# Performance work log

Hardware: AMD Instinct MI355X
Metric: run time of the kernel (lower is better)

## Reference

```python
import jax, jax.numpy as jnp
import numpy as np

N_TOK, EMBED, N_CLS, BATCH, N_HEAD = 32768, 512, 16, 8, 8
D_HEAD = EMBED // N_HEAD


def setup_inputs() -> dict:
    key0 = jax.random.key(0)
    ks = jax.random.split(key0, 12)
    s = 1.0 / np.sqrt(EMBED)
    query = jax.random.normal(ks[0], (N_TOK, EMBED), dtype=jnp.float32)
    key_f = jax.random.normal(ks[1], (N_CLS, BATCH, EMBED), dtype=jnp.float32)
    val_f = jax.random.normal(ks[2], (N_CLS, BATCH, EMBED), dtype=jnp.float32)
    batch_idx = jnp.sort(jax.random.randint(ks[3], (N_TOK,), 0, BATCH)).astype(jnp.int32)
    Wq = jax.random.normal(ks[4], (EMBED, EMBED), dtype=jnp.float32) * s
    bq = jnp.zeros((EMBED,), dtype=jnp.float32)
    Wk = jax.random.normal(ks[5], (EMBED, EMBED), dtype=jnp.float32) * s  # Conv1d(k=1) kernel squeezed
    bk = jnp.zeros((EMBED,), dtype=jnp.float32)
    Wv = jax.random.normal(ks[6], (EMBED, EMBED), dtype=jnp.float32) * s
    bv = jnp.zeros((EMBED,), dtype=jnp.float32)
    Wo = jax.random.normal(ks[7], (EMBED, EMBED), dtype=jnp.float32) * s
    bo = jnp.zeros((EMBED,), dtype=jnp.float32)
    return {"query": query, "key": key_f, "value": val_f, "batch_idx": batch_idx,
            "batch_size": BATCH, "Wq": Wq, "bq": bq, "Wk": Wk, "bk": bk,
            "Wv": Wv, "bv": bv, "Wo": Wo, "bo": bo}


def reference(query, key, value, batch_idx, batch_size, Wq, bq, Wk, bk, Wv, bv, Wo, bo):
    n_tok, embed = query.shape
    L, B, _ = key.shape
    H, D = N_HEAD, EMBED // N_HEAD
    scale = D ** -0.5  # matmul_norm
    # projections (Conv1d with kernel_size=1 == pointwise linear over E)
    q = (query @ Wq.T + bq).reshape(n_tok, H, D)                           # [N,H,D]
    k = (jnp.einsum('lbe,fe->blf', key, Wk) + bk)                          # [B,L,E]
    k = k.transpose(0, 2, 1).reshape(B, H, D, L)                           # [B,H,D,L]
    v = (jnp.einsum('lbe,fe->blf', value, Wv) + bv)                        # [B,L,E]
    v = v.transpose(0, 2, 1).reshape(B, H, D, L).transpose(0, 1, 3, 2)     # [B,H,L,D]
    # scores against every batch's prototypes, then pick each token's batch
    scores_all = jnp.einsum('nhd,bhdl->nbhl', q, k) * scale                # [N,B,H,L]
    sel = batch_idx.astype(jnp.int32)[:, None, None, None]
    scores = jnp.take_along_axis(scores_all, sel, axis=1).squeeze(1)       # [N,H,L]
    p = jax.nn.softmax(scores, axis=-1)
    ctx_all = jnp.einsum('nhl,bhld->nbhd', p, v)                           # [N,B,H,D]
    ctx = jnp.take_along_axis(ctx_all, sel, axis=1).squeeze(1)             # [N,H,D]
    return ctx.reshape(n_tok, embed) @ Wo.T + bo
```

## Files before the change

kernel.cpp:

```cpp
#include <hip/hip_runtime.h>

typedef unsigned short u16;
typedef __attribute__((ext_vector_type(8))) short short8;
typedef __attribute__((ext_vector_type(4))) unsigned short u16x4;
typedef __attribute__((ext_vector_type(4))) float f32x4;

#define N_TOKENS 32768
#define EMBED 512
#define NCLS 16
#define NBATCH 8
#define NHEAD 8
#define DHEAD 64

__device__ __forceinline__ u16 f2bf(float f) {
  unsigned u = __float_as_uint(f);
  u += 0x7fffu + ((u >> 16) & 1u);
  return (u16)(u >> 16);
}

__device__ __forceinline__ void async16(const u16* g, u16* l) {
  __builtin_amdgcn_global_load_lds(
      (__attribute__((address_space(1))) const unsigned int*)(const void*)g,
      (__attribute__((address_space(3))) unsigned int*)(void*)l,
      16, 0, 0);
}

__global__ __launch_bounds__(256) void kvproj_kernel(
    const float* __restrict__ key, const float* __restrict__ val,
    const float* __restrict__ Wk, const float* __restrict__ bk,
    const float* __restrict__ Wv, const float* __restrict__ bv,
    float* __restrict__ kproj, float* __restrict__ vproj) {
  int t = blockIdx.x * blockDim.x + threadIdx.x;
  int o = t >> 1;
  int half = t & 1;
  const bool isV = o >= 65536;
  int idx = o & 65535;
  int f = idx & 511;
  int bl = idx >> 9;
  int l = bl & 15;
  int b = bl >> 4;
  const float* src = isV ? val : key;
  const float* W = isV ? Wv : Wk;
  const float* bias = isV ? bv : bk;
  const float4* s4 = (const float4*)(src + (size_t)l * (NBATCH * EMBED) + (size_t)b * EMBED) + half * 64;
  const float4* w4 = (const float4*)(W + (size_t)f * EMBED) + half * 64;
  float acc = 0.f;
#pragma unroll 8
  for (int e = 0; e < 64; e++) {
    float4 a = s4[e], w = w4[e];
    acc += a.x * w.x + a.y * w.y + a.z * w.z + a.w * w.w;
  }
  acc += __shfl_xor(acc, 1);
  if (half == 0) {
    acc += bias[f];
    if (!isV) {
      kproj[((size_t)(b * EMBED + f)) * NCLS + l] = acc;
    } else {
      int h = f >> 6, d = f & 63;
      vproj[(size_t)b * 8192 + (size_t)h * 1024 + l * 64 + d] = acc;
    }
  }
}

__global__ __launch_bounds__(256) void build_all(
    const float* __restrict__ kproj, const float* __restrict__ vproj,
    const float* __restrict__ Wq, const float* __restrict__ bq,
    const float* __restrict__ Wo,
    u16* __restrict__ Kqb, u16* __restrict__ WoVb, float* __restrict__ sb) {
  const int blk = blockIdx.x;
  if (blk < 2048) {
    int t = blk * 256 + threadIdx.x;
    int e = t & 511;
    int hl = (t >> 9) & 127;
    int b = t >> 16;
    int h = hl >> 4, l = hl & 15;
    const float* kp = kproj + (size_t)b * 8192 + h * 1024 + l;
    const float* wq = Wq + (size_t)(h * 64) * 512 + e;
    float acc = 0.f;
#pragma unroll 16
    for (int d = 0; d < 64; d++) acc += kp[d * 16] * wq[d * 512];
    Kqb[t] = f2bf(acc);
  } else if (blk < 4096) {
    int t = (blk - 2048) * 256 + threadIdx.x;
    int hl = t & 127;
    int f = (t >> 7) & 511;
    int b = t >> 16;
    int h = hl >> 4, l = hl & 15;
    const float* vp = vproj + (size_t)b * 8192 + h * 1024 + l * 64;
    const float* wo = Wo + (size_t)f * 512 + h * 64;
    float acc = 0.f;
#pragma unroll 16
    for (int d = 0; d < 64; d++) acc += vp[d] * wo[d];
    WoVb[t] = f2bf(acc);
  } else {
    int t = (blk - 4096) * 256 + threadIdx.x;
    int hl = t & 127, b = t >> 7;
    int h = hl >> 4, l = hl & 15;
    const float* kp = kproj + (size_t)b * 8192 + h * 1024 + l;
    const float* q = bq + h * 64;
    float acc = 0.f;
#pragma unroll
    for (int d = 0; d < 64; d++) acc += q[d] * kp[d * 16];
    sb[t] = acc;
  }
}

__global__ __launch_bounds__(256) void fused_attn(
    const float* __restrict__ query, const u16* __restrict__ Kqb,
    const u16* __restrict__ WoVb, const float* __restrict__ sb,
    const float* __restrict__ bo, const int* __restrict__ bidx,
    float* __restrict__ out) {
  __shared__ __align__(16) u16 Bs[2][128 * 32];
  __shared__ __align__(16) u16 Ps[64 * 128];
  const int tid = threadIdx.x;
  const int lane = tid & 63;
  const int wave = tid >> 6;
  const int quad = lane >> 4;
  const int l16 = lane & 15;
  const int tileId = blockIdx.x >> 1;
  const int slot = blockIdx.x & 1;
  const int m0 = tileId * 64;
  const int bFirst = bidx[m0];
  const int bLast = bidx[m0 + 63];
  if (slot == 1 && bFirst == bLast) return;
  const int b0 = (slot == 0) ? bFirst : bFirst + 1;
  const int b1 = (slot == 0) ? bFirst : bLast;

  const int r0 = tid >> 2, r1 = r0 + 64;
  const int lg0 = (tid & 3) ^ ((r0 >> 1) & 3);
  const int lg1 = (tid & 3) ^ ((r1 >> 1) & 3);
  const size_t boff0 = (size_t)r0 * 512 + lg0 * 8;
  const size_t boff1 = (size_t)r1 * 512 + lg1 * 8;

  int rowb[4][4];
#pragma unroll
  for (int mi = 0; mi < 4; mi++)
#pragma unroll
    for (int r = 0; r < 4; r++) rowb[mi][r] = bidx[m0 + mi * 16 + quad * 4 + r];

  const float* pA = query + (size_t)(m0 + wave * 16 + l16) * 512 + quad * 8;

  for (int bb = b0; bb <= b1; bb++) {
    const u16* Bq = Kqb + (size_t)bb * 65536;

    async16(Bq + boff0, &Bs[0][tid * 8]);
    async16(Bq + boff1, &Bs[0][tid * 8 + 2048]);
    float4 na0 = *(const float4*)(pA);
    float4 na1 = *(const float4*)(pA + 4);

    f32x4 acc1[8];
#pragma unroll
    for (int j = 0; j < 8; j++) acc1[j] = (f32x4){0.f, 0.f, 0.f, 0.f};

    for (int t = 0; t < 16; t++) {
      __syncthreads();
      const int cur = t & 1;
      if (t < 15) {
        const int ko = (t + 1) * 32;
        async16(Bq + boff0 + ko, &Bs[cur ^ 1][tid * 8]);
        async16(Bq + boff1 + ko, &Bs[cur ^ 1][tid * 8 + 2048]);
      }
      float4 a0 = na0, a1 = na1;
      if (t < 15) {
        na0 = *(const float4*)(pA + (t + 1) * 32);
        na1 = *(const float4*)(pA + (t + 1) * 32 + 4);
      }
      short8 af;
      af[0] = (short)f2bf(a0.x); af[1] = (short)f2bf(a0.y);
      af[2] = (short)f2bf(a0.z); af[3] = (short)f2bf(a0.w);
      af[4] = (short)f2bf(a1.x); af[5] = (short)f2bf(a1.y);
      af[6] = (short)f2bf(a1.z); af[7] = (short)f2bf(a1.w);
#pragma unroll
      for (int ni = 0; ni < 8; ni++) {
        const int rw = ni * 16 + l16;
        short8 bfr = *(const short8*)&Bs[cur][rw * 32 + ((quad ^ ((rw >> 1) & 3)) << 3)];
        acc1[ni] = __builtin_amdgcn_mfma_f32_16x16x32_bf16(af, bfr, acc1[ni], 0, 0, 0);
      }
    }

    float sbv[8];
#pragma unroll
    for (int ni = 0; ni < 8; ni++) sbv[ni] = sb[bb * 128 + ni * 16 + l16];
#pragma unroll
    for (int r = 0; r < 4; r++) {
      const int row = wave * 16 + quad * 4 + r;
#pragma unroll
      for (int ni = 0; ni < 8; ni++) {
        float v = acc1[ni][r] + sbv[ni];
        float mx = v;
        mx = fmaxf(mx, __shfl_xor(mx, 1));
        mx = fmaxf(mx, __shfl_xor(mx, 2));
        mx = fmaxf(mx, __shfl_xor(mx, 4));
        mx = fmaxf(mx, __shfl_xor(mx, 8));
        float ev = __expf((v - mx) * 0.125f);
        float s = ev;
        s += __shfl_xor(s, 1);
        s += __shfl_xor(s, 2);
        s += __shfl_xor(s, 4);
        s += __shfl_xor(s, 8);
        const int col = ni * 16 + l16;
        Ps[row * 128 + (((col >> 3) ^ (row & 7)) << 3) + (col & 7)] = f2bf(ev / s);
      }
    }
    __syncthreads();

    const u16* Wv = WoVb + (size_t)bb * 65536;
#pragma unroll
    for (int h2 = 0; h2 < 2; h2++) {
      const int f0 = wave * 128 + h2 * 64;
      f32x4 acc2[4][4];
#pragma unroll
      for (int i = 0; i < 4; i++)
#pragma unroll
        for (int j = 0; j < 4; j++) acc2[i][j] = (f32x4){0.f, 0.f, 0.f, 0.f};
#pragma unroll
      for (int kk = 0; kk < 4; kk++) {
        short8 paf[4], bf2[4];
#pragma unroll
        for (int mi = 0; mi < 4; mi++) {
          const int row = mi * 16 + l16;
          paf[mi] = *(const short8*)&Ps[row * 128 + (((kk * 4 + quad) ^ (row & 7)) << 3)];
        }
#pragma unroll
        for (int ni = 0; ni < 4; ni++) {
          const int fr = f0 + ni * 16 + l16;
          bf2[ni] = *(const short8*)(Wv + (size_t)fr * 128 + kk * 32 + quad * 8);
        }
#pragma unroll
        for (int mi = 0; mi < 4; mi++)
#pragma unroll
          for (int ni = 0; ni < 4; ni++)
            acc2[mi][ni] = __builtin_amdgcn_mfma_f32_16x16x32_bf16(paf[mi], bf2[ni], acc2[mi][ni], 0, 0, 0);
      }
      float bov[4];
#pragma unroll
      for (int ni = 0; ni < 4; ni++) bov[ni] = bo[f0 + ni * 16 + l16];
#pragma unroll
      for (int mi = 0; mi < 4; mi++)
#pragma unroll
        for (int r = 0; r < 4; r++) {
          if (rowb[mi][r] == bb) {
            const size_t row = m0 + mi * 16 + quad * 4 + r;
#pragma unroll
            for (int ni = 0; ni < 4; ni++)
              out[row * 512 + f0 + ni * 16 + l16] = acc2[mi][ni][r] + bov[ni];
          }
        }
    }
    __syncthreads();
  }
}

extern "C" void kernel_launch(void* const* d_in, const int* in_sizes, int n_in,
                              void* d_out, int out_size, void* d_ws, size_t ws_size,
                              hipStream_t stream) {
  const float* query = (const float*)d_in[0];
  const float* keyt = (const float*)d_in[1];
  const float* valt = (const float*)d_in[2];
  const int* bidx = (const int*)d_in[3];
  const float* Wq = (const float*)d_in[5];
  const float* bq = (const float*)d_in[6];
  const float* Wk = (const float*)d_in[7];
  const float* bk = (const float*)d_in[8];
  const float* Wv = (const float*)d_in[9];
  const float* bv = (const float*)d_in[10];
  const float* Wo = (const float*)d_in[11];
  const float* bo = (const float*)d_in[12];
  float* out = (float*)d_out;

  unsigned char* w = (unsigned char*)d_ws;
  float* kproj = (float*)(w + 41943040ull);
  float* vproj = (float*)(w + 42205184ull);
  u16* Kqb = (u16*)(w + 42467328ull);
  u16* WoVb = (u16*)(w + 43515904ull);
  float* sb = (float*)(w + 44564480ull);

  kvproj_kernel<<<1024, 256, 0, stream>>>(keyt, valt, Wk, bk, Wv, bv, kproj, vproj);

  build_all<<<4100, 256, 0, stream>>>(kproj, vproj, Wq, bq, Wo, Kqb, WoVb, sb);

  fused_attn<<<N_TOKENS / 64 * 2, 256, 0, stream>>>(query, Kqb, WoVb, sb, bo, bidx, out);
}
```

Baseline: 277.3 us.

## Load Kq fragments directly from global, rework K/V projection and WoV build reductions

```diff
diff --git a/kernel.cpp b/kernel.cpp
--- a/kernel.cpp
+++ b/kernel.cpp
@@ -18,46 +18,42 @@
   return (u16)(u >> 16);
 }
 
-__device__ __forceinline__ void async16(const u16* g, u16* l) {
-  __builtin_amdgcn_global_load_lds(
-      (__attribute__((address_space(1))) const unsigned int*)(const void*)g,
-      (__attribute__((address_space(3))) unsigned int*)(void*)l,
-      16, 0, 0);
-}
-
 __global__ __launch_bounds__(256) void kvproj_kernel(
     const float* __restrict__ key, const float* __restrict__ val,
     const float* __restrict__ Wk, const float* __restrict__ bk,
     const float* __restrict__ Wv, const float* __restrict__ bv,
     float* __restrict__ kproj, float* __restrict__ vproj) {
-  int t = blockIdx.x * blockDim.x + threadIdx.x;
-  int o = t >> 1;
-  int half = t & 1;
-  const bool isV = o >= 65536;
-  int idx = o & 65535;
-  int f = idx & 511;
-  int bl = idx >> 9;
-  int l = bl & 15;
-  int b = bl >> 4;
+  const int tid = threadIdx.x;
+  const bool isV = blockIdx.x & 1;
+  const int fgrp = blockIdx.x >> 1;
+  const int wave = tid >> 6;
+  const int ec = tid & 63;
+  const int fr = fgrp * 4 + wave;
+  const float* W = (isV ? Wv : Wk) + (size_t)fr * 512 + ec * 8;
+  const float4 w0 = *(const float4*)W;
+  const float4 w1 = *(const float4*)(W + 4);
   const float* src = isV ? val : key;
-  const float* W = isV ? Wv : Wk;
-  const float* bias = isV ? bv : bk;
-  const float4* s4 = (const float4*)(src + (size_t)l * (NBATCH * EMBED) + (size_t)b * EMBED) + half * 64;
-  const float4* w4 = (const float4*)(W + (size_t)f * EMBED) + half * 64;
-  float acc = 0.f;
-#pragma unroll 8
-  for (int e = 0; e < 64; e++) {
-    float4 a = s4[e], w = w4[e];
-    acc += a.x * w.x + a.y * w.y + a.z * w.z + a.w * w.w;
-  }
-  acc += __shfl_xor(acc, 1);
-  if (half == 0) {
-    acc += bias[f];
-    if (!isV) {
-      kproj[((size_t)(b * EMBED + f)) * NCLS + l] = acc;
-    } else {
-      int h = f >> 6, d = f & 63;
-      vproj[(size_t)b * 8192 + (size_t)h * 1024 + l * 64 + d] = acc;
+  const float bval = (isV ? bv : bk)[fr];
+  const int h = fr >> 6, d = fr & 63;
+
+#pragma unroll 4
+  for (int r = 0; r < 128; r++) {
+    const int b = r >> 4, l = r & 15;
+    const float* s = src + (size_t)l * (NBATCH * EMBED) + (size_t)b * EMBED + ec * 8;
+    float4 a0 = *(const float4*)s;
+    float4 a1 = *(const float4*)(s + 4);
+    float acc = a0.x * w0.x + a0.y * w0.y + a0.z * w0.z + a0.w * w0.w +
+                a1.x * w1.x + a1.y * w1.y + a1.z * w1.z + a1.w * w1.w;
+    acc += __shfl_xor(acc, 1);
+    acc += __shfl_xor(acc, 2);
+    acc += __shfl_xor(acc, 4);
+    acc += __shfl_xor(acc, 8);
+    acc += __shfl_xor(acc, 16);
+    acc += __shfl_xor(acc, 32);
+    if (ec == 0) {
+      acc += bval;
+      if (!isV) kproj[((size_t)(b * EMBED + fr)) * NCLS + l] = acc;
+      else      vproj[(size_t)b * 8192 + (size_t)h * 1024 + l * 64 + d] = acc;
     }
   }
 }
@@ -80,20 +76,32 @@
 #pragma unroll 16
     for (int d = 0; d < 64; d++) acc += kp[d * 16] * wq[d * 512];
     Kqb[t] = f2bf(acc);
-  } else if (blk < 4096) {
-    int t = (blk - 2048) * 256 + threadIdx.x;
-    int hl = t & 127;
-    int f = (t >> 7) & 511;
-    int b = t >> 16;
-    int h = hl >> 4, l = hl & 15;
-    const float* vp = vproj + (size_t)b * 8192 + h * 1024 + l * 64;
-    const float* wo = Wo + (size_t)f * 512 + h * 64;
-    float acc = 0.f;
-#pragma unroll 16
-    for (int d = 0; d < 64; d++) acc += vp[d] * wo[d];
-    WoVb[t] = f2bf(acc);
+  } else if (blk < 3072) {
+    const int wave = threadIdx.x >> 6;
+    const int lane = threadIdx.x & 63;
+    const int wgid = (blk - 2048) * 4 + wave;
+    const int b = wgid >> 9, f = wgid & 511;
+    const int l = lane >> 2, c = lane & 3;
+    const float* vp = vproj + (size_t)b * 8192 + l * 64 + c * 16;
+    const float* wo = Wo + (size_t)f * 512 + c * 16;
+#pragma unroll 2
+    for (int h = 0; h < 8; h++) {
+      const float* v = vp + h * 1024;
+      const float* w = wo + h * 64;
+      float4 v0 = *(const float4*)v,       w0 = *(const float4*)w;
+      float4 v1 = *(const float4*)(v + 4), w1 = *(const float4*)(w + 4);
+      float4 v2 = *(const float4*)(v + 8), w2 = *(const float4*)(w + 8);
+      float4 v3 = *(const float4*)(v + 12), w3 = *(const float4*)(w + 12);
+      float acc = v0.x * w0.x + v0.y * w0.y + v0.z * w0.z + v0.w * w0.w +
+                  v1.x * w1.x + v1.y * w1.y + v1.z * w1.z + v1.w * w1.w +
+                  v2.x * w2.x + v2.y * w2.y + v2.z * w2.z + v2.w * w2.w +
+                  v3.x * w3.x + v3.y * w3.y + v3.z * w3.z + v3.w * w3.w;
+      acc += __shfl_xor(acc, 1);
+      acc += __shfl_xor(acc, 2);
+      if (c == 0) WoVb[(size_t)b * 65536 + (size_t)f * 128 + h * 16 + l] = f2bf(acc);
+    }
   } else {
-    int t = (blk - 4096) * 256 + threadIdx.x;
+    int t = (blk - 3072) * 256 + threadIdx.x;
     int hl = t & 127, b = t >> 7;
     int h = hl >> 4, l = hl & 15;
     const float* kp = kproj + (size_t)b * 8192 + h * 1024 + l;
@@ -110,7 +118,6 @@
     const u16* __restrict__ WoVb, const float* __restrict__ sb,
     const float* __restrict__ bo, const int* __restrict__ bidx,
     float* __restrict__ out) {
-  __shared__ __align__(16) u16 Bs[2][128 * 32];
   __shared__ __align__(16) u16 Ps[64 * 128];
   const int tid = threadIdx.x;
   const int lane = tid & 63;
@@ -126,12 +133,6 @@
   const int b0 = (slot == 0) ? bFirst : bFirst + 1;
   const int b1 = (slot == 0) ? bFirst : bLast;
 
-  const int r0 = tid >> 2, r1 = r0 + 64;
-  const int lg0 = (tid & 3) ^ ((r0 >> 1) & 3);
-  const int lg1 = (tid & 3) ^ ((r1 >> 1) & 3);
-  const size_t boff0 = (size_t)r0 * 512 + lg0 * 8;
-  const size_t boff1 = (size_t)r1 * 512 + lg1 * 8;
-
   int rowb[4][4];
 #pragma unroll
   for (int mi = 0; mi < 4; mi++)
@@ -141,40 +142,42 @@
   const float* pA = query + (size_t)(m0 + wave * 16 + l16) * 512 + quad * 8;
 
   for (int bb = b0; bb <= b1; bb++) {
-    const u16* Bq = Kqb + (size_t)bb * 65536;
-
-    async16(Bq + boff0, &Bs[0][tid * 8]);
-    async16(Bq + boff1, &Bs[0][tid * 8 + 2048]);
-    float4 na0 = *(const float4*)(pA);
-    float4 na1 = *(const float4*)(pA + 4);
+    const u16* Bq = Kqb + (size_t)bb * 65536 + (size_t)l16 * 512 + quad * 8;
 
     f32x4 acc1[8];
 #pragma unroll
     for (int j = 0; j < 8; j++) acc1[j] = (f32x4){0.f, 0.f, 0.f, 0.f};
 
+    short8 bc[8];
+#pragma unroll
+    for (int ni = 0; ni < 8; ni++)
+      bc[ni] = *(const short8*)(Bq + (size_t)ni * 16 * 512);
+    float4 a0c = *(const float4*)pA;
+    float4 a1c = *(const float4*)(pA + 4);
+
+#pragma unroll
     for (int t = 0; t < 16; t++) {
-      __syncthreads();
-      const int cur = t & 1;
+      short8 bn[8];
+      float4 a0n, a1n;
       if (t < 15) {
-        const int ko = (t + 1) * 32;
-        async16(Bq + boff0 + ko, &Bs[cur ^ 1][tid * 8]);
-        async16(Bq + boff1 + ko, &Bs[cur ^ 1][tid * 8 + 2048]);
-      }
-      float4 a0 = na0, a1 = na1;
+#pragma unroll
+        for (int ni = 0; ni < 8; ni++)
+          bn[ni] = *(const short8*)(Bq + (size_t)ni * 16 * 512 + (t + 1) * 32);
+        a0n = *(const float4*)(pA + (t + 1) * 32);
+        a1n = *(const float4*)(pA + (t + 1) * 32 + 4);
+      }
+      short8 af;
+      af[0] = (short)f2bf(a0c.x); af[1] = (short)f2bf(a0c.y);
+      af[2] = (short)f2bf(a0c.z); af[3] = (short)f2bf(a0c.w);
+      af[4] = (short)f2bf(a1c.x); af[5] = (short)f2bf(a1c.y);
+      af[6] = (short)f2bf(a1c.z); af[7] = (short)f2bf(a1c.w);
+#pragma unroll
+      for (int ni = 0; ni < 8; ni++)
+        acc1[ni] = __builtin_amdgcn_mfma_f32_16x16x32_bf16(af, bc[ni], acc1[ni], 0, 0, 0);
       if (t < 15) {
-        na0 = *(const float4*)(pA + (t + 1) * 32);
-        na1 = *(const float4*)(pA + (t + 1) * 32 + 4);
-      }
-      short8 af;
-      af[0] = (short)f2bf(a0.x); af[1] = (short)f2bf(a0.y);
-      af[2] = (short)f2bf(a0.z); af[3] = (short)f2bf(a0.w);
-      af[4] = (short)f2bf(a1.x); af[5] = (short)f2bf(a1.y);
-      af[6] = (short)f2bf(a1.z); af[7] = (short)f2bf(a1.w);
-#pragma unroll
-      for (int ni = 0; ni < 8; ni++) {
-        const int rw = ni * 16 + l16;
-        short8 bfr = *(const short8*)&Bs[cur][rw * 32 + ((quad ^ ((rw >> 1) & 3)) << 3)];
-        acc1[ni] = __builtin_amdgcn_mfma_f32_16x16x32_bf16(af, bfr, acc1[ni], 0, 0, 0);
+#pragma unroll
+        for (int ni = 0; ni < 8; ni++) bc[ni] = bn[ni];
+        a0c = a0n; a1c = a1n;
       }
     }
 
@@ -275,9 +278,9 @@
   u16* WoVb = (u16*)(w + 43515904ull);
   float* sb = (float*)(w + 44564480ull);
 
-  kvproj_kernel<<<1024, 256, 0, stream>>>(keyt, valt, Wk, bk, Wv, bv, kproj, vproj);
-
-  build_all<<<4100, 256, 0, stream>>>(kproj, vproj, Wq, bq, Wo, Kqb, WoVb, sb);
+  kvproj_kernel<<<256, 256, 0, stream>>>(keyt, valt, Wk, bk, Wv, bv, kproj, vproj);
+
+  build_all<<<3076, 256, 0, stream>>>(kproj, vproj, Wq, bq, Wo, Kqb, WoVb, sb);
 
   fused_attn<<<N_TOKENS / 64 * 2, 256, 0, stream>>>(query, Kqb, WoVb, sb, bo, bidx, out);
 }
```

Result: slower. 326.9 us (+17.9%).
